# Optimization experiments

Measured on AMD Instinct MI355X. Metric: run time of the kernel, lower is better.

Reference implementation:

```python
import jax, jax.numpy as jnp
import numpy as np

B, M, P, W = 128, 10000, 64, 24


def setup_inputs() -> dict:
    key = jax.random.key(0)
    k1, k2, k3 = jax.random.split(key, 3)
    x = jax.random.normal(k1, (B, M, P), dtype=jnp.float32)
    weight = jax.random.normal(k2, (M, P, W), dtype=jnp.float32)
    bound = 1.0 / np.sqrt(P)
    bias = jax.random.uniform(k3, (M, W), dtype=jnp.float32, minval=-bound, maxval=bound)
    return {"x": x, "weight": weight, "bias": bias}


def reference(x, weight, bias):
    # Per-channel linear: out[b, w, j] = sum_p x[b, j, p] * weight[j, p, w] + bias[j, w]
    # Replaces the original python loop of m tiny GEMMs with one batched contraction.
    out = jnp.einsum('bjp,jpw->bwj', x, weight) + bias.T[None, :, :]  # [B, W, M]
    return out
```

## Files before the change

kernel.cpp:

```cpp
#include <hip/hip_runtime.h>


constexpr int B  = 128;
constexpr int M  = 10000;
constexpr int P  = 64;
constexpr int W  = 24;

constexpr int JT  = 16;
constexpr int BH  = 16;
constexpr int NCH = 4;
constexpr int NT  = 1024;
constexpr int NWG = (M / JT) * (B / (BH * NCH));

using bf8   = __attribute__((ext_vector_type(8))) __bf16;
using bf4   = __attribute__((ext_vector_type(4))) __bf16;
using f32x4 = __attribute__((ext_vector_type(4))) float;

__global__ __launch_bounds__(NT, 4) void pcl_kernel(
    const float* __restrict__ x, const float* __restrict__ wgt,
    const float* __restrict__ bias, float* __restrict__ out) {
  __shared__ __align__(16) char smem[32768];
  unsigned short* xsh  = reinterpret_cast<unsigned short*>(smem);
  float*          obuf = reinterpret_cast<float*>(smem);

  const int t = threadIdx.x;

  const int orig = blockIdx.x;
  const int xcd  = orig & 7;
  const int idx  = orig >> 3;
  const int wgid = (xcd < 2 ? xcd * 157 : 314 + (xcd - 2) * 156) + idx;
  const int jt    = wgid >> 1;
  const int bbase = (wgid & 1) * (BH * NCH);
  const int j0    = jt * JT;

  const int wk   = t >> 6;
  const int lane = t & 63;
  const int col  = lane & 15;
  const int kg   = lane >> 4;
  const int j    = j0 + wk;

  float bv[2];
#pragma unroll
  for (int nt = 0; nt < 2; ++nt) {
    const int w = nt * 16 + col;
    bv[nt] = (w < W) ? bias[(size_t)j * W + w] : 0.0f;
  }

  bf8 bfr[2][2];
#pragma unroll
  for (int ks = 0; ks < 2; ++ks) {
#pragma unroll
    for (int nt = 0; nt < 2; ++nt) {
      const int w     = nt * 16 + col;
      const bool ok   = (w < W);
      const float* wp = wgt + (size_t)j * (P * W) +
                        (size_t)(ks * 32 + kg * 8) * W + (ok ? w : 0);
      bf8 v;
#pragma unroll
      for (int e = 0; e < 8; ++e) v[e] = (__bf16)wp[(size_t)e * W];
      if (!ok) {
#pragma unroll
        for (int e = 0; e < 8; ++e) v[e] = (__bf16)0.0f;
      }
      bfr[ks][nt] = v;
    }
  }

  float4 nx[4];
#pragma unroll
  for (int i = 0; i < 4; ++i) {
    const int g  = t + i * NT;
    const int b  = g >> 8;
    const int jj = (g >> 4) & 15;
    const int c2 = g & 15;
    nx[i] = *reinterpret_cast<const float4*>(
        x + ((size_t)(bbase + b) * M + j0 + jj) * P + 4 * c2);
  }

  for (int c = 0; c < NCH; ++c) {
    if (c > 0) __syncthreads();

#pragma unroll
    for (int i = 0; i < 4; ++i) {
      const int g  = t + i * NT;
      const int b  = g >> 8;
      const int jj = (g >> 4) & 15;
      const int c2 = g & 15;
      bf4 v;
      v[0] = (__bf16)nx[i].x; v[1] = (__bf16)nx[i].y;
      v[2] = (__bf16)nx[i].z; v[3] = (__bf16)nx[i].w;
      const int s = (c2 >> 1) ^ (b & 7);
      *reinterpret_cast<bf4*>(xsh + (((b << 4) + jj) << 6) + (s << 3) +
                              ((c2 & 1) << 2)) = v;
    }

    if (c < NCH - 1) {
      const int b0n = bbase + (c + 1) * BH;
#pragma unroll
      for (int i = 0; i < 4; ++i) {
        const int g  = t + i * NT;
        const int b  = g >> 8;
        const int jj = (g >> 4) & 15;
        const int c2 = g & 15;
        nx[i] = *reinterpret_cast<const float4*>(
            x + ((size_t)(b0n + b) * M + j0 + jj) * P + 4 * c2);
      }
    }

    __syncthreads();

    f32x4 acc[2];
#pragma unroll
    for (int nt = 0; nt < 2; ++nt)
      acc[nt] = f32x4{bv[nt], bv[nt], bv[nt], bv[nt]};

#pragma unroll
    for (int ks = 0; ks < 2; ++ks) {
      const int cc = ks * 4 + kg;
      const bf8 af = *reinterpret_cast<const bf8*>(
          xsh + (((col << 4) + wk) << 6) + ((cc ^ (col & 7)) << 3));
#pragma unroll
      for (int nt = 0; nt < 2; ++nt)
        acc[nt] = __builtin_amdgcn_mfma_f32_16x16x32_bf16(
            af, bfr[ks][nt], acc[nt], 0, 0, 0);
    }

    __syncthreads();

#pragma unroll
    for (int nt = 0; nt < 2; ++nt) {
      const int w = nt * 16 + col;
      if (w < W) {
#pragma unroll
        for (int reg = 0; reg < 4; ++reg)
          obuf[(wk * 16 + kg * 4 + reg) * 25 + w] = acc[nt][reg];
      }
    }
    __syncthreads();

    const int b0c = bbase + c * BH;
#pragma unroll
    for (int it = 0; it < 2; ++it) {
      const int d = t + it * NT;
      if (d < 1536) {
        const int jq   = d & 3;
        const int rest = d >> 2;
        const int w    = rest % 24;
        const int br   = rest / 24;
        float4 o;
        o.x = obuf[((4 * jq + 0) * 16 + br) * 25 + w];
        o.y = obuf[((4 * jq + 1) * 16 + br) * 25 + w];
        o.z = obuf[((4 * jq + 2) * 16 + br) * 25 + w];
        o.w = obuf[((4 * jq + 3) * 16 + br) * 25 + w];
        *reinterpret_cast<float4*>(
            out + ((size_t)(b0c + br) * W + w) * M + j0 + 4 * jq) = o;
      }
    }
  }
}

extern "C" void kernel_launch(void* const* d_in, const int* in_sizes, int n_in,
                              void* d_out, int out_size, void* d_ws, size_t ws_size,
                              hipStream_t stream) {
  const float* x    = (const float*)d_in[0];
  const float* wgt  = (const float*)d_in[1];
  const float* bias = (const float*)d_in[2];
  float* out        = (float*)d_out;

  dim3 grid(NWG);
  dim3 block(NT);
  hipLaunchKernelGGL(pcl_kernel, grid, block, 0, stream, x, wgt, bias, out);
}
```

Before: 111.7 us.

## Separate output staging buffer from x tile to cut barriers per chunk

Moves the output staging buffer to its own LDS region so it no longer aliases the x tile. The next chunk's x tile can then be written right after the output staging barrier, and the global prefetch runs two chunks ahead. This drops the per-chunk barrier count from four to two. The cost is LDS use rising from 32KB to about 57KB per workgroup, which may lower occupancy from the 4 workgroups per CU requested in launch bounds.

```diff
diff --git a/kernel.cpp b/kernel.cpp
--- a/kernel.cpp
+++ b/kernel.cpp
@@ -19,9 +19,9 @@
 __global__ __launch_bounds__(NT, 4) void pcl_kernel(
     const float* __restrict__ x, const float* __restrict__ wgt,
     const float* __restrict__ bias, float* __restrict__ out) {
-  __shared__ __align__(16) char smem[32768];
+  __shared__ __align__(16) char smem[58368];
   unsigned short* xsh  = reinterpret_cast<unsigned short*>(smem);
-  float*          obuf = reinterpret_cast<float*>(smem);
+  float*          obuf = reinterpret_cast<float*>(smem + 32768);
 
   const int t = threadIdx.x;
 
@@ -66,49 +66,39 @@
     }
   }
 
+  const int gb  = t >> 8;
+  const int gj  = (t >> 4) & 15;
+  const int gc2 = t & 15;
+
   float4 nx[4];
 #pragma unroll
   for (int i = 0; i < 4; ++i) {
-    const int g  = t + i * NT;
-    const int b  = g >> 8;
-    const int jj = (g >> 4) & 15;
-    const int c2 = g & 15;
     nx[i] = *reinterpret_cast<const float4*>(
-        x + ((size_t)(bbase + b) * M + j0 + jj) * P + 4 * c2);
+        x + ((size_t)(bbase + gb + 4 * i) * M + j0 + gj) * P + 4 * gc2);
   }
 
-  for (int c = 0; c < NCH; ++c) {
-    if (c > 0) __syncthreads();
-
+  {
+    const int s = (gc2 >> 1) ^ (gb & 7);
 #pragma unroll
     for (int i = 0; i < 4; ++i) {
-      const int g  = t + i * NT;
-      const int b  = g >> 8;
-      const int jj = (g >> 4) & 15;
-      const int c2 = g & 15;
+      const int b = gb + 4 * i;
+      const int ss = (gc2 >> 1) ^ (b & 7);
       bf4 v;
       v[0] = (__bf16)nx[i].x; v[1] = (__bf16)nx[i].y;
       v[2] = (__bf16)nx[i].z; v[3] = (__bf16)nx[i].w;
-      const int s = (c2 >> 1) ^ (b & 7);
-      *reinterpret_cast<bf4*>(xsh + (((b << 4) + jj) << 6) + (s << 3) +
-                              ((c2 & 1) << 2)) = v;
+      *reinterpret_cast<bf4*>(xsh + (((b << 4) + gj) << 6) + (ss << 3) +
+                              ((gc2 & 1) << 2)) = v;
     }
+    (void)s;
+#pragma unroll
+    for (int i = 0; i < 4; ++i) {
+      nx[i] = *reinterpret_cast<const float4*>(
+          x + ((size_t)(bbase + BH + gb + 4 * i) * M + j0 + gj) * P + 4 * gc2);
+    }
+  }
+  __syncthreads();
 
-    if (c < NCH - 1) {
-      const int b0n = bbase + (c + 1) * BH;
-#pragma unroll
-      for (int i = 0; i < 4; ++i) {
-        const int g  = t + i * NT;
-        const int b  = g >> 8;
-        const int jj = (g >> 4) & 15;
-        const int c2 = g & 15;
-        nx[i] = *reinterpret_cast<const float4*>(
-            x + ((size_t)(b0n + b) * M + j0 + jj) * P + 4 * c2);
-      }
-    }
-
-    __syncthreads();
-
+  for (int c = 0; c < NCH; ++c) {
     f32x4 acc[2];
 #pragma unroll
     for (int nt = 0; nt < 2; ++nt)
@@ -125,8 +115,6 @@
             af, bfr[ks][nt], acc[nt], 0, 0, 0);
     }
 
-    __syncthreads();
-
 #pragma unroll
     for (int nt = 0; nt < 2; ++nt) {
       const int w = nt * 16 + col;
@@ -137,6 +125,27 @@
       }
     }
     __syncthreads();
+
+    if (c < NCH - 1) {
+#pragma unroll
+      for (int i = 0; i < 4; ++i) {
+        const int b = gb + 4 * i;
+        const int ss = (gc2 >> 1) ^ (b & 7);
+        bf4 v;
+        v[0] = (__bf16)nx[i].x; v[1] = (__bf16)nx[i].y;
+        v[2] = (__bf16)nx[i].z; v[3] = (__bf16)nx[i].w;
+        *reinterpret_cast<bf4*>(xsh + (((b << 4) + gj) << 6) + (ss << 3) +
+                                ((gc2 & 1) << 2)) = v;
+      }
+      if (c < NCH - 2) {
+        const int b0n = bbase + (c + 2) * BH;
+#pragma unroll
+        for (int i = 0; i < 4; ++i) {
+          nx[i] = *reinterpret_cast<const float4*>(
+              x + ((size_t)(b0n + gb + 4 * i) * M + j0 + gj) * P + 4 * gc2);
+        }
+      }
+    }
 
     const int b0c = bbase + c * BH;
 #pragma unroll
@@ -156,6 +165,8 @@
             out + ((size_t)(b0c + br) * W + w) * M + j0 + 4 * jq) = o;
       }
     }
+    if (c < NCH - 1)
+      __syncthreads();
   }
 }
 
```

New measurement: 113.8 us. No clear change (+1.8%).
